# Kernel optimization log

Measured on AMD Instinct MI355X. Metric: run time of the kernel, lower is better.

The kernel has to match this reference:

```python
import jax, jax.numpy as jnp
import numpy as np

N_NODES = 100000
N_EDGES = 1600000
Z_DIM = 64
EDGE_FEAT_DIM = 16
HIDDEN = 128


def setup_inputs() -> dict:
    key = jax.random.key(0)
    k_z, k_ei, k_ea, k_w1, k_b1, k_w2, k_b2 = jax.random.split(key, 7)
    in_dim = 2 * Z_DIM + EDGE_FEAT_DIM
    return {
        "z": jax.random.normal(k_z, (N_NODES, Z_DIM), dtype=jnp.float32),
        "edge_index": jax.random.randint(k_ei, (2, N_EDGES), 0, N_NODES, dtype=jnp.int64),
        "edge_attr": jax.random.normal(k_ea, (N_EDGES, EDGE_FEAT_DIM), dtype=jnp.float32),
        # decoder_mlp params: Linear(2*z_dim+edge_feat_dim, 128) -> ReLU -> Linear(128, 1)
        "W1": jax.random.normal(k_w1, (in_dim, HIDDEN), dtype=jnp.float32) / np.float32(np.sqrt(in_dim)),
        "b1": jax.random.normal(k_b1, (HIDDEN,), dtype=jnp.float32) * 0.01,
        "W2": jax.random.normal(k_w2, (HIDDEN, 1), dtype=jnp.float32) / np.float32(np.sqrt(HIDDEN)),
        "b2": jax.random.normal(k_b2, (1,), dtype=jnp.float32) * 0.01,
    }


def reference(z, edge_index, edge_attr, W1, b1, W2, b2):
    # decode(): gather endpoint embeddings, concat edge features, 2-layer MLP, sigmoid
    src = edge_index[0]
    dst = edge_index[1]
    edge_input = jnp.concatenate([z[src], z[dst], edge_attr], axis=1)  # [E, 2Z+F]
    h = jax.nn.relu(edge_input @ W1 + b1)  # [E, 128]
    logits = h @ W2 + b2                   # [E, 1]
    return jax.nn.sigmoid(logits).squeeze(-1)  # [E]
```

## Files before the change

kernel.cpp:

```cpp
#include <hip/hip_runtime.h>

#define EDGES 1600000
#define NN    100000
#define ZD    64
#define FD    16
#define HID   128
#define BM    32
#define THREADS 256
#define NBLK  1250
#define TPW   10
#define NFRAG 2560
#define WT_SHORTS (NFRAG * 8)

typedef __attribute__((ext_vector_type(8)))  short bfrag;
typedef __attribute__((ext_vector_type(16))) float f16v;

__device__ __forceinline__ unsigned short f2bf(float f) {
  unsigned u = __builtin_bit_cast(unsigned, f);
  u += 0x7fffu + ((u >> 16) & 1u);
  return (unsigned short)(u >> 16);
}
__device__ __forceinline__ unsigned cvtpk(float lo, float hi) {
  unsigned r;
  asm("v_cvt_pk_bf16_f32 %0, %1, %2" : "=v"(r) : "v"(lo), "v"(hi));
  return r;
}
__device__ __forceinline__ void gload16(const void* g, void* l) {
  __builtin_amdgcn_global_load_lds(
      (const __attribute__((address_space(1))) unsigned int*)g,
      (__attribute__((address_space(3))) unsigned int*)l, 16, 0, 0);
}

__global__ void zconv_kernel(const float* __restrict__ z,
                             unsigned short* __restrict__ z16, int n4) {
  int i = blockIdx.x * blockDim.x + threadIdx.x;
  if (i >= n4) return;
  float4 f = reinterpret_cast<const float4*>(z)[i];
  ushort4 p;
  p.x = f2bf(f.x); p.y = f2bf(f.y); p.z = f2bf(f.z); p.w = f2bf(f.w);
  reinterpret_cast<ushort4*>(z16)[i] = p;
}

__global__ void wtab_kernel(const float* __restrict__ W1,
                            const float* __restrict__ b1,
                            unsigned short* __restrict__ WT) {
  int i = blockIdx.x * blockDim.x + threadIdx.x;
  if (i >= WT_SHORTS) return;
  int j    = i & 7;
  int frag = i >> 3;
  int lane = frag & 63;
  int s    = (frag >> 6) % 10;
  int blk  = frag / 640;
  int hid  = blk * 32 + (lane & 31);
  int k    = s * 16 + (lane >> 5) * 8 + j;
  float v = (k < 144) ? W1[k * HID + hid] : (k == 144 ? b1[hid] : 0.f);
  WT[i] = f2bf(v);
}

template<bool ZB>
__global__ __launch_bounds__(THREADS, 2) void fused_kernel(
    const float* __restrict__ zf, const unsigned short* __restrict__ z16,
    const unsigned short* __restrict__ WT,
    const int* __restrict__ ei, const float* __restrict__ ea,
    const float* __restrict__ W2, const float* __restrict__ b2,
    float* __restrict__ out)
{
  __shared__ __align__(16) int4 sW[NFRAG];
  __shared__ __align__(16) float sW2[HID];

  const int tid  = threadIdx.x;
  const int lane = tid & 63;
  const int wid  = tid >> 6;
  const int e    = lane & 31;
  const int hi   = lane >> 5;

  #pragma unroll
  for (int c = 0; c < 10; ++c)
    gload16(WT + (size_t)(c * 256 + tid) * 8, &sW[c * 256 + tid]);
  if (tid < HID) sW2[tid] = W2[tid];
  asm volatile("s_waitcnt vmcnt(0)" ::: "memory");
  __syncthreads();

  const float bias2 = b2[0];

  int4 oq = {0, 0, 0, 0};
  if (hi == 0) oq.x = 0x3F80;
  const bfrag cone = __builtin_bit_cast(bfrag, oq);

  f16v zerov;
  #pragma unroll
  for (int rg = 0; rg < 16; ++rg) zerov[rg] = 0.f;

#define GZ(x0, x1, x2, x3, x4, x5, x6, x7, xa, xb, si, di, tt) do {            \
    if constexpr (ZB) {                                                        \
      const unsigned short* ps_ = z16 + (size_t)(si) * ZD + hi * 8;            \
      const unsigned short* pd_ = z16 + (size_t)(di) * ZD + hi * 8;            \
      x0 = *reinterpret_cast<const bfrag*>(ps_);                               \
      x1 = *reinterpret_cast<const bfrag*>(ps_ + 16);                          \
      x2 = *reinterpret_cast<const bfrag*>(ps_ + 32);                          \
      x3 = *reinterpret_cast<const bfrag*>(ps_ + 48);                          \
      x4 = *reinterpret_cast<const bfrag*>(pd_);                               \
      x5 = *reinterpret_cast<const bfrag*>(pd_ + 16);                          \
      x6 = *reinterpret_cast<const bfrag*>(pd_ + 32);                          \
      x7 = *reinterpret_cast<const bfrag*>(pd_ + 48);                          \
    } else {                                                                   \
      const float* ps_ = zf + (size_t)(si) * ZD + hi * 8;                      \
      const float* pd_ = zf + (size_t)(di) * ZD + hi * 8;                      \
      float4 a_, b_;                                                           \
      a_ = ((const float4*)ps_)[0]; b_ = ((const float4*)ps_)[1];              \
      { int4 q_ = {(int)cvtpk(a_.x,a_.y),(int)cvtpk(a_.z,a_.w),                \
                   (int)cvtpk(b_.x,b_.y),(int)cvtpk(b_.z,b_.w)};               \
        x0 = __builtin_bit_cast(bfrag, q_); }                                  \
      a_ = ((const float4*)(ps_+16))[0]; b_ = ((const float4*)(ps_+16))[1];    \
      { int4 q_ = {(int)cvtpk(a_.x,a_.y),(int)cvtpk(a_.z,a_.w),                \
                   (int)cvtpk(b_.x,b_.y),(int)cvtpk(b_.z,b_.w)};               \
        x1 = __builtin_bit_cast(bfrag, q_); }                                  \
      a_ = ((const float4*)(ps_+32))[0]; b_ = ((const float4*)(ps_+32))[1];    \
      { int4 q_ = {(int)cvtpk(a_.x,a_.y),(int)cvtpk(a_.z,a_.w),                \
                   (int)cvtpk(b_.x,b_.y),(int)cvtpk(b_.z,b_.w)};               \
        x2 = __builtin_bit_cast(bfrag, q_); }                                  \
      a_ = ((const float4*)(ps_+48))[0]; b_ = ((const float4*)(ps_+48))[1];    \
      { int4 q_ = {(int)cvtpk(a_.x,a_.y),(int)cvtpk(a_.z,a_.w),                \
                   (int)cvtpk(b_.x,b_.y),(int)cvtpk(b_.z,b_.w)};               \
        x3 = __builtin_bit_cast(bfrag, q_); }                                  \
      a_ = ((const float4*)pd_)[0]; b_ = ((const float4*)pd_)[1];              \
      { int4 q_ = {(int)cvtpk(a_.x,a_.y),(int)cvtpk(a_.z,a_.w),                \
                   (int)cvtpk(b_.x,b_.y),(int)cvtpk(b_.z,b_.w)};               \
        x4 = __builtin_bit_cast(bfrag, q_); }                                  \
      a_ = ((const float4*)(pd_+16))[0]; b_ = ((const float4*)(pd_+16))[1];    \
      { int4 q_ = {(int)cvtpk(a_.x,a_.y),(int)cvtpk(a_.z,a_.w),                \
                   (int)cvtpk(b_.x,b_.y),(int)cvtpk(b_.z,b_.w)};               \
        x5 = __builtin_bit_cast(bfrag, q_); }                                  \
      a_ = ((const float4*)(pd_+32))[0]; b_ = ((const float4*)(pd_+32))[1];    \
      { int4 q_ = {(int)cvtpk(a_.x,a_.y),(int)cvtpk(a_.z,a_.w),                \
                   (int)cvtpk(b_.x,b_.y),(int)cvtpk(b_.z,b_.w)};               \
        x6 = __builtin_bit_cast(bfrag, q_); }                                  \
      a_ = ((const float4*)(pd_+48))[0]; b_ = ((const float4*)(pd_+48))[1];    \
      { int4 q_ = {(int)cvtpk(a_.x,a_.y),(int)cvtpk(a_.z,a_.w),                \
                   (int)cvtpk(b_.x,b_.y),(int)cvtpk(b_.z,b_.w)};               \
        x7 = __builtin_bit_cast(bfrag, q_); }                                  \
    }                                                                          \
    const float* pe_ = ea + ((size_t)(tt) * BM + e) * FD + hi * 8;             \
    xa = ((const float4*)pe_)[0];                                              \
    xb = ((const float4*)pe_)[1];                                              \
  } while (0)

  const int gw = blockIdx.x * 4 + wid;
  const int T0 = gw * TPW;

  int si = ei[(size_t)T0 * BM + e];
  int di = ei[(size_t)EDGES + (size_t)T0 * BM + e];
  bfrag c0, c1, c2, c3, c4, c5, c6, c7; float4 ca, cb;
  GZ(c0, c1, c2, c3, c4, c5, c6, c7, ca, cb, si, di, T0);
  int s1 = ei[(size_t)(T0 + 1) * BM + e];
  int d1 = ei[(size_t)EDGES + (size_t)(T0 + 1) * BM + e];

  for (int t = 0; t < TPW; ++t) {
    const int tt = T0 + t;

    const int tn = (t + 1 < TPW) ? tt + 1 : tt;
    bfrag n0, n1, n2, n3, n4, n5, n6, n7; float4 na, nb;
    GZ(n0, n1, n2, n3, n4, n5, n6, n7, na, nb, s1, d1, tn);

    const int tf = (t + 2 < TPW) ? tt + 2 : T0 + TPW - 1;
    s1 = ei[(size_t)tf * BM + e];
    d1 = ei[(size_t)EDGES + (size_t)tf * BM + e];

    int4 eq = {(int)cvtpk(ca.x, ca.y), (int)cvtpk(ca.z, ca.w),
               (int)cvtpk(cb.x, cb.y), (int)cvtpk(cb.z, cb.w)};
    bfrag c8 = __builtin_bit_cast(bfrag, eq);

    __builtin_amdgcn_s_setprio(1);
    float p0 = 0.f, p1 = 0.f, p2 = 0.f, p3 = 0.f;
    #pragma unroll
    for (int blk = 0; blk < 4; ++blk) {
      const int4* wp = &sW[blk * 640 + lane];

      bfrag w0 = *reinterpret_cast<const bfrag*>(wp + 0 * 64);
      bfrag w2 = *reinterpret_cast<const bfrag*>(wp + 2 * 64);
      bfrag w4 = *reinterpret_cast<const bfrag*>(wp + 4 * 64);
      bfrag w6 = *reinterpret_cast<const bfrag*>(wp + 6 * 64);
      bfrag w8 = *reinterpret_cast<const bfrag*>(wp + 8 * 64);
      f16v accA;
      accA = __builtin_amdgcn_mfma_f32_32x32x16_bf16(w0, c0, zerov, 0, 0, 0);
      accA = __builtin_amdgcn_mfma_f32_32x32x16_bf16(w2, c2, accA, 0, 0, 0);
      accA = __builtin_amdgcn_mfma_f32_32x32x16_bf16(w4, c4, accA, 0, 0, 0);
      accA = __builtin_amdgcn_mfma_f32_32x32x16_bf16(w6, c6, accA, 0, 0, 0);
      accA = __builtin_amdgcn_mfma_f32_32x32x16_bf16(w8, c8, accA, 0, 0, 0);

      bfrag w9 = *reinterpret_cast<const bfrag*>(wp + 9 * 64);
      bfrag w1 = *reinterpret_cast<const bfrag*>(wp + 1 * 64);
      bfrag w3 = *reinterpret_cast<const bfrag*>(wp + 3 * 64);
      bfrag w5 = *reinterpret_cast<const bfrag*>(wp + 5 * 64);
      bfrag w7 = *reinterpret_cast<const bfrag*>(wp + 7 * 64);
      f16v accB;
      accB = __builtin_amdgcn_mfma_f32_32x32x16_bf16(w9, cone, zerov, 0, 0, 0);
      accB = __builtin_amdgcn_mfma_f32_32x32x16_bf16(w1, c1, accB, 0, 0, 0);
      accB = __builtin_amdgcn_mfma_f32_32x32x16_bf16(w3, c3, accB, 0, 0, 0);
      accB = __builtin_amdgcn_mfma_f32_32x32x16_bf16(w5, c5, accB, 0, 0, 0);
      accB = __builtin_amdgcn_mfma_f32_32x32x16_bf16(w7, c7, accB, 0, 0, 0);

      const float* wq = &sW2[blk * 32 + 4 * hi];
      float4 q0 = *reinterpret_cast<const float4*>(wq);
      float4 q1 = *reinterpret_cast<const float4*>(wq + 8);
      float4 q2 = *reinterpret_cast<const float4*>(wq + 16);
      float4 q3 = *reinterpret_cast<const float4*>(wq + 24);

      p0 = fmaf(fmaxf(accA[0]  + accB[0],  0.f), q0.x, p0);
      p1 = fmaf(fmaxf(accA[1]  + accB[1],  0.f), q0.y, p1);
      p2 = fmaf(fmaxf(accA[2]  + accB[2],  0.f), q0.z, p2);
      p3 = fmaf(fmaxf(accA[3]  + accB[3],  0.f), q0.w, p3);
      p0 = fmaf(fmaxf(accA[4]  + accB[4],  0.f), q1.x, p0);
      p1 = fmaf(fmaxf(accA[5]  + accB[5],  0.f), q1.y, p1);
      p2 = fmaf(fmaxf(accA[6]  + accB[6],  0.f), q1.z, p2);
      p3 = fmaf(fmaxf(accA[7]  + accB[7],  0.f), q1.w, p3);
      p0 = fmaf(fmaxf(accA[8]  + accB[8],  0.f), q2.x, p0);
      p1 = fmaf(fmaxf(accA[9]  + accB[9],  0.f), q2.y, p1);
      p2 = fmaf(fmaxf(accA[10] + accB[10], 0.f), q2.z, p2);
      p3 = fmaf(fmaxf(accA[11] + accB[11], 0.f), q2.w, p3);
      p0 = fmaf(fmaxf(accA[12] + accB[12], 0.f), q3.x, p0);
      p1 = fmaf(fmaxf(accA[13] + accB[13], 0.f), q3.y, p1);
      p2 = fmaf(fmaxf(accA[14] + accB[14], 0.f), q3.z, p2);
      p3 = fmaf(fmaxf(accA[15] + accB[15], 0.f), q3.w, p3);
    }
    __builtin_amdgcn_s_setprio(0);

    float p = (p0 + p1) + (p2 + p3);
    p += __shfl_xor(p, 32);
    if (lane < 32)
      out[(size_t)tt * BM + lane] = 1.f / (1.f + __expf(-(p + bias2)));

    c0 = n0; c1 = n1; c2 = n2; c3 = n3;
    c4 = n4; c5 = n5; c6 = n6; c7 = n7;
    ca = na; cb = nb;
  }
#undef GZ
}

extern "C" void kernel_launch(void* const* d_in, const int* in_sizes, int n_in,
                              void* d_out, int out_size, void* d_ws, size_t ws_size,
                              hipStream_t stream) {
  const float* z  = (const float*)d_in[0];
  const int*   ei = (const int*)d_in[1];
  const float* ea = (const float*)d_in[2];
  const float* W1 = (const float*)d_in[3];
  const float* b1 = (const float*)d_in[4];
  const float* W2 = (const float*)d_in[5];
  const float* b2 = (const float*)d_in[6];
  float* out = (float*)d_out;

  const size_t z16_bytes = (size_t)NN * ZD * sizeof(unsigned short);
  const size_t wt_bytes  = (size_t)WT_SHORTS * sizeof(unsigned short);

  if (ws_size >= z16_bytes + wt_bytes) {
    unsigned short* z16 = (unsigned short*)d_ws;
    unsigned short* WT  = z16 + (size_t)NN * ZD;
    const int n4 = NN * ZD / 4;
    zconv_kernel<<<(n4 + 255) / 256, 256, 0, stream>>>(z, z16, n4);
    wtab_kernel<<<(WT_SHORTS + 255) / 256, 256, 0, stream>>>(W1, b1, WT);
    fused_kernel<true><<<NBLK, THREADS, 0, stream>>>(
        z, z16, WT, ei, ea, W2, b2, out);
  } else {
    unsigned short* WT = (unsigned short*)d_ws;
    wtab_kernel<<<(WT_SHORTS + 255) / 256, 256, 0, stream>>>(W1, b1, WT);
    fused_kernel<false><<<NBLK, THREADS, 0, stream>>>(
        z, nullptr, WT, ei, ea, W2, b2, out);
  }
}
```

Measured before the change: 94.14 us.

## Process 64-edge tiles per wave, sharing LDS weight fragments across two chains

Each wave now handles 64 edges per iteration as two 32-edge halves. Each half runs its own full-K MFMA accumulation chain, so one set of W1 fragments read from LDS serves both halves and LDS weight traffic per edge drops by half. The per-wave work is kept the same by halving TPW. The previous software prefetch of the next tile's z and edge_attr gathers is removed; only the next tile's edge indices are prefetched. Gather latency must now be hidden by occupancy and the two independent chains, and each MFMA chain is longer.

```diff
diff --git a/kernel.cpp b/kernel.cpp
--- a/kernel.cpp
+++ b/kernel.cpp
@@ -5,10 +5,11 @@
 #define ZD    64
 #define FD    16
 #define HID   128
-#define BM    32
+#define BM    64
 #define THREADS 256
 #define NBLK  1250
-#define TPW   10
+#define TPW   5
+#define KSTEPS 10
 #define NFRAG 2560
 #define WT_SHORTS (NFRAG * 8)
 
@@ -49,8 +50,8 @@
   int j    = i & 7;
   int frag = i >> 3;
   int lane = frag & 63;
-  int s    = (frag >> 6) % 10;
-  int blk  = frag / 640;
+  int s    = (frag >> 6) % KSTEPS;
+  int blk  = frag / (KSTEPS * 64);
   int hid  = blk * 32 + (lane & 31);
   int k    = s * 16 + (lane >> 5) * 8 + j;
   float v = (k < 144) ? W1[k * HID + hid] : (k == 144 ? b1[hid] : 0.f);
@@ -91,7 +92,7 @@
   #pragma unroll
   for (int rg = 0; rg < 16; ++rg) zerov[rg] = 0.f;
 
-#define GZ(x0, x1, x2, x3, x4, x5, x6, x7, xa, xb, si, di, tt) do {            \
+#define GZ(x0, x1, x2, x3, x4, x5, x6, x7, xa, xb, si, di, ebase) do {         \
     if constexpr (ZB) {                                                        \
       const unsigned short* ps_ = z16 + (size_t)(si) * ZD + hi * 8;            \
       const unsigned short* pd_ = z16 + (size_t)(di) * ZD + hi * 8;            \
@@ -140,7 +141,7 @@
                    (int)cvtpk(b_.x,b_.y),(int)cvtpk(b_.z,b_.w)};               \
         x7 = __builtin_bit_cast(bfrag, q_); }                                  \
     }                                                                          \
-    const float* pe_ = ea + ((size_t)(tt) * BM + e) * FD + hi * 8;             \
+    const float* pe_ = ea + (size_t)(ebase) * FD + hi * 8;                     \
     xa = ((const float4*)pe_)[0];                                              \
     xb = ((const float4*)pe_)[1];                                              \
   } while (0)
@@ -148,91 +149,125 @@
   const int gw = blockIdx.x * 4 + wid;
   const int T0 = gw * TPW;
 
-  int si = ei[(size_t)T0 * BM + e];
-  int di = ei[(size_t)EDGES + (size_t)T0 * BM + e];
-  bfrag c0, c1, c2, c3, c4, c5, c6, c7; float4 ca, cb;
-  GZ(c0, c1, c2, c3, c4, c5, c6, c7, ca, cb, si, di, T0);
-  int s1 = ei[(size_t)(T0 + 1) * BM + e];
-  int d1 = ei[(size_t)EDGES + (size_t)(T0 + 1) * BM + e];
+  int sA = ei[(size_t)T0 * BM + e];
+  int dA = ei[(size_t)EDGES + (size_t)T0 * BM + e];
+  int sB = ei[(size_t)T0 * BM + 32 + e];
+  int dB = ei[(size_t)EDGES + (size_t)T0 * BM + 32 + e];
 
   for (int t = 0; t < TPW; ++t) {
     const int tt = T0 + t;
 
-    const int tn = (t + 1 < TPW) ? tt + 1 : tt;
-    bfrag n0, n1, n2, n3, n4, n5, n6, n7; float4 na, nb;
-    GZ(n0, n1, n2, n3, n4, n5, n6, n7, na, nb, s1, d1, tn);
-
-    const int tf = (t + 2 < TPW) ? tt + 2 : T0 + TPW - 1;
-    s1 = ei[(size_t)tf * BM + e];
-    d1 = ei[(size_t)EDGES + (size_t)tf * BM + e];
-
-    int4 eq = {(int)cvtpk(ca.x, ca.y), (int)cvtpk(ca.z, ca.w),
-               (int)cvtpk(cb.x, cb.y), (int)cvtpk(cb.z, cb.w)};
-    bfrag c8 = __builtin_bit_cast(bfrag, eq);
+    bfrag a0, a1, a2, a3, a4, a5, a6, a7; float4 aa, ab;
+    GZ(a0, a1, a2, a3, a4, a5, a6, a7, aa, ab, sA, dA, (size_t)tt * BM + e);
+    bfrag g0, g1, g2, g3, g4, g5, g6, g7; float4 ga, gb;
+    GZ(g0, g1, g2, g3, g4, g5, g6, g7, ga, gb, sB, dB, (size_t)tt * BM + 32 + e);
+
+    {
+      const int tn = (t + 1 < TPW) ? tt + 1 : tt;
+      sA = ei[(size_t)tn * BM + e];
+      dA = ei[(size_t)EDGES + (size_t)tn * BM + e];
+      sB = ei[(size_t)tn * BM + 32 + e];
+      dB = ei[(size_t)EDGES + (size_t)tn * BM + 32 + e];
+    }
+
+    int4 eqa = {(int)cvtpk(aa.x, aa.y), (int)cvtpk(aa.z, aa.w),
+                (int)cvtpk(ab.x, ab.y), (int)cvtpk(ab.z, ab.w)};
+    bfrag a8 = __builtin_bit_cast(bfrag, eqa);
+    int4 eqb = {(int)cvtpk(ga.x, ga.y), (int)cvtpk(ga.z, ga.w),
+                (int)cvtpk(gb.x, gb.y), (int)cvtpk(gb.z, gb.w)};
+    bfrag g8 = __builtin_bit_cast(bfrag, eqb);
 
     __builtin_amdgcn_s_setprio(1);
     float p0 = 0.f, p1 = 0.f, p2 = 0.f, p3 = 0.f;
+    float q0 = 0.f, q1 = 0.f, q2 = 0.f, q3 = 0.f;
     #pragma unroll
     for (int blk = 0; blk < 4; ++blk) {
-      const int4* wp = &sW[blk * 640 + lane];
-
+      const int4* wp = &sW[blk * (KSTEPS * 64) + lane];
       bfrag w0 = *reinterpret_cast<const bfrag*>(wp + 0 * 64);
+      bfrag w1 = *reinterpret_cast<const bfrag*>(wp + 1 * 64);
       bfrag w2 = *reinterpret_cast<const bfrag*>(wp + 2 * 64);
+      bfrag w3 = *reinterpret_cast<const bfrag*>(wp + 3 * 64);
       bfrag w4 = *reinterpret_cast<const bfrag*>(wp + 4 * 64);
+      bfrag w5 = *reinterpret_cast<const bfrag*>(wp + 5 * 64);
       bfrag w6 = *reinterpret_cast<const bfrag*>(wp + 6 * 64);
+      bfrag w7 = *reinterpret_cast<const bfrag*>(wp + 7 * 64);
       bfrag w8 = *reinterpret_cast<const bfrag*>(wp + 8 * 64);
+      bfrag w9 = *reinterpret_cast<const bfrag*>(wp + 9 * 64);
+
       f16v accA;
-      accA = __builtin_amdgcn_mfma_f32_32x32x16_bf16(w0, c0, zerov, 0, 0, 0);
-      accA = __builtin_amdgcn_mfma_f32_32x32x16_bf16(w2, c2, accA, 0, 0, 0);
-      accA = __builtin_amdgcn_mfma_f32_32x32x16_bf16(w4, c4, accA, 0, 0, 0);
-      accA = __builtin_amdgcn_mfma_f32_32x32x16_bf16(w6, c6, accA, 0, 0, 0);
-      accA = __builtin_amdgcn_mfma_f32_32x32x16_bf16(w8, c8, accA, 0, 0, 0);
-
-      bfrag w9 = *reinterpret_cast<const bfrag*>(wp + 9 * 64);
-      bfrag w1 = *reinterpret_cast<const bfrag*>(wp + 1 * 64);
-      bfrag w3 = *reinterpret_cast<const bfrag*>(wp + 3 * 64);
-      bfrag w5 = *reinterpret_cast<const bfrag*>(wp + 5 * 64);
-      bfrag w7 = *reinterpret_cast<const bfrag*>(wp + 7 * 64);
+      accA = __builtin_amdgcn_mfma_f32_32x32x16_bf16(w9, cone, zerov, 0, 0, 0);
+      accA = __builtin_amdgcn_mfma_f32_32x32x16_bf16(w0, a0, accA, 0, 0, 0);
+      accA = __builtin_amdgcn_mfma_f32_32x32x16_bf16(w1, a1, accA, 0, 0, 0);
+      accA = __builtin_amdgcn_mfma_f32_32x32x16_bf16(w2, a2, accA, 0, 0, 0);
+      accA = __builtin_amdgcn_mfma_f32_32x32x16_bf16(w3, a3, accA, 0, 0, 0);
+      accA = __builtin_amdgcn_mfma_f32_32x32x16_bf16(w4, a4, accA, 0, 0, 0);
+      accA = __builtin_amdgcn_mfma_f32_32x32x16_bf16(w5, a5, accA, 0, 0, 0);
+      accA = __builtin_amdgcn_mfma_f32_32x32x16_bf16(w6, a6, accA, 0, 0, 0);
+      accA = __builtin_amdgcn_mfma_f32_32x32x16_bf16(w7, a7, accA, 0, 0, 0);
+      accA = __builtin_amdgcn_mfma_f32_32x32x16_bf16(w8, a8, accA, 0, 0, 0);
+
       f16v accB;
       accB = __builtin_amdgcn_mfma_f32_32x32x16_bf16(w9, cone, zerov, 0, 0, 0);
-      accB = __builtin_amdgcn_mfma_f32_32x32x16_bf16(w1, c1, accB, 0, 0, 0);
-      accB = __builtin_amdgcn_mfma_f32_32x32x16_bf16(w3, c3, accB, 0, 0, 0);
-      accB = __builtin_amdgcn_mfma_f32_32x32x16_bf16(w5, c5, accB, 0, 0, 0);
-      accB = __builtin_amdgcn_mfma_f32_32x32x16_bf16(w7, c7, accB, 0, 0, 0);
+      accB = __builtin_amdgcn_mfma_f32_32x32x16_bf16(w0, g0, accB, 0, 0, 0);
+      accB = __builtin_amdgcn_mfma_f32_32x32x16_bf16(w1, g1, accB, 0, 0, 0);
+      accB = __builtin_amdgcn_mfma_f32_32x32x16_bf16(w2, g2, accB, 0, 0, 0);
+      accB = __builtin_amdgcn_mfma_f32_32x32x16_bf16(w3, g3, accB, 0, 0, 0);
+      accB = __builtin_amdgcn_mfma_f32_32x32x16_bf16(w4, g4, accB, 0, 0, 0);
+      accB = __builtin_amdgcn_mfma_f32_32x32x16_bf16(w5, g5, accB, 0, 0, 0);
+      accB = __builtin_amdgcn_mfma_f32_32x32x16_bf16(w6, g6, accB, 0, 0, 0);
+      accB = __builtin_amdgcn_mfma_f32_32x32x16_bf16(w7, g7, accB, 0, 0, 0);
+      accB = __builtin_amdgcn_mfma_f32_32x32x16_bf16(w8, g8, accB, 0, 0, 0);
 
       const float* wq = &sW2[blk * 32 + 4 * hi];
-      float4 q0 = *reinterpret_cast<const float4*>(wq);
-      float4 q1 = *reinterpret_cast<const float4*>(wq + 8);
-      float4 q2 = *reinterpret_cast<const float4*>(wq + 16);
-      float4 q3 = *reinterpret_cast<const float4*>(wq + 24);
-
-      p0 = fmaf(fmaxf(accA[0]  + accB[0],  0.f), q0.x, p0);
-      p1 = fmaf(fmaxf(accA[1]  + accB[1],  0.f), q0.y, p1);
-      p2 = fmaf(fmaxf(accA[2]  + accB[2],  0.f), q0.z, p2);
-      p3 = fmaf(fmaxf(accA[3]  + accB[3],  0.f), q0.w, p3);
-      p0 = fmaf(fmaxf(accA[4]  + accB[4],  0.f), q1.x, p0);
-      p1 = fmaf(fmaxf(accA[5]  + accB[5],  0.f), q1.y, p1);
-      p2 = fmaf(fmaxf(accA[6]  + accB[6],  0.f), q1.z, p2);
-      p3 = fmaf(fmaxf(accA[7]  + accB[7],  0.f), q1.w, p3);
-      p0 = fmaf(fmaxf(accA[8]  + accB[8],  0.f), q2.x, p0);
-      p1 = fmaf(fmaxf(accA[9]  + accB[9],  0.f), q2.y, p1);
-      p2 = fmaf(fmaxf(accA[10] + accB[10], 0.f), q2.z, p2);
-      p3 = fmaf(fmaxf(accA[11] + accB[11], 0.f), q2.w, p3);
-      p0 = fmaf(fmaxf(accA[12] + accB[12], 0.f), q3.x, p0);
-      p1 = fmaf(fmaxf(accA[13] + accB[13], 0.f), q3.y, p1);
-      p2 = fmaf(fmaxf(accA[14] + accB[14], 0.f), q3.z, p2);
-      p3 = fmaf(fmaxf(accA[15] + accB[15], 0.f), q3.w, p3);
+      float4 c0_ = *reinterpret_cast<const float4*>(wq);
+      float4 c1_ = *reinterpret_cast<const float4*>(wq + 8);
+      float4 c2_ = *reinterpret_cast<const float4*>(wq + 16);
+      float4 c3_ = *reinterpret_cast<const float4*>(wq + 24);
+
+      p0 = fmaf(fmaxf(accA[0],  0.f), c0_.x, p0);
+      p1 = fmaf(fmaxf(accA[1],  0.f), c0_.y, p1);
+      p2 = fmaf(fmaxf(accA[2],  0.f), c0_.z, p2);
+      p3 = fmaf(fmaxf(accA[3],  0.f), c0_.w, p3);
+      p0 = fmaf(fmaxf(accA[4],  0.f), c1_.x, p0);
+      p1 = fmaf(fmaxf(accA[5],  0.f), c1_.y, p1);
+      p2 = fmaf(fmaxf(accA[6],  0.f), c1_.z, p2);
+      p3 = fmaf(fmaxf(accA[7],  0.f), c1_.w, p3);
+      p0 = fmaf(fmaxf(accA[8],  0.f), c2_.x, p0);
+      p1 = fmaf(fmaxf(accA[9],  0.f), c2_.y, p1);
+      p2 = fmaf(fmaxf(accA[10], 0.f), c2_.z, p2);
+      p3 = fmaf(fmaxf(accA[11], 0.f), c2_.w, p3);
+      p0 = fmaf(fmaxf(accA[12], 0.f), c3_.x, p0);
+      p1 = fmaf(fmaxf(accA[13], 0.f), c3_.y, p1);
+      p2 = fmaf(fmaxf(accA[14], 0.f), c3_.z, p2);
+      p3 = fmaf(fmaxf(accA[15], 0.f), c3_.w, p3);
+
+      q0 = fmaf(fmaxf(accB[0],  0.f), c0_.x, q0);
+      q1 = fmaf(fmaxf(accB[1],  0.f), c0_.y, q1);
+      q2 = fmaf(fmaxf(accB[2],  0.f), c0_.z, q2);
+      q3 = fmaf(fmaxf(accB[3],  0.f), c0_.w, q3);
+      q0 = fmaf(fmaxf(accB[4],  0.f), c1_.x, q0);
+      q1 = fmaf(fmaxf(accB[5],  0.f), c1_.y, q1);
+      q2 = fmaf(fmaxf(accB[6],  0.f), c1_.z, q2);
+      q3 = fmaf(fmaxf(accB[7],  0.f), c1_.w, q3);
+      q0 = fmaf(fmaxf(accB[8],  0.f), c2_.x, q0);
+      q1 = fmaf(fmaxf(accB[9],  0.f), c2_.y, q1);
+      q2 = fmaf(fmaxf(accB[10], 0.f), c2_.z, q2);
+      q3 = fmaf(fmaxf(accB[11], 0.f), c2_.w, q3);
+      q0 = fmaf(fmaxf(accB[12], 0.f), c3_.x, q0);
+      q1 = fmaf(fmaxf(accB[13], 0.f), c3_.y, q1);
+      q2 = fmaf(fmaxf(accB[14], 0.f), c3_.z, q2);
+      q3 = fmaf(fmaxf(accB[15], 0.f), c3_.w, q3);
     }
     __builtin_amdgcn_s_setprio(0);
 
     float p = (p0 + p1) + (p2 + p3);
     p += __shfl_xor(p, 32);
-    if (lane < 32)
-      out[(size_t)tt * BM + lane] = 1.f / (1.f + __expf(-(p + bias2)));
-
-    c0 = n0; c1 = n1; c2 = n2; c3 = n3;
-    c4 = n4; c5 = n5; c6 = n6; c7 = n7;
-    ca = na; cb = nb;
+    float q = (q0 + q1) + (q2 + q3);
+    q += __shfl_xor(q, 32);
+    if (lane < 32) {
+      out[(size_t)tt * BM + lane]      = 1.f / (1.f + __expf(-(p + bias2)));
+      out[(size_t)tt * BM + 32 + lane] = 1.f / (1.f + __expf(-(q + bias2)));
+    }
   }
 #undef GZ
 }
```

Result: slower. 98.36 us (+4.5%).
